# Kernel optimization log

Measured on AMD Instinct MI355X. Metric: run time of the kernel, lower is better.

The kernel has to match this reference:

```python
import jax, jax.numpy as jnp
import numpy as np

B, N = 32, 1000
HID, COM = 256, 64
T_LEN, NOP = 288, 3
NVAL, TP_D, CS_D, TIME_D = 9, 2, 4, 4
IN_C = CS_D + TP_D + NVAL            # 15, competition GAT input
IN_CO = IN_C + COM                    # 79, cooperation GAT input
OBS = TIME_D + TP_D + CS_D + 2 * COM + NVAL  # 147
K_D = K_F = 500                       # int(0.5*N + 0.5)
TEMP = 1.0
NEG = jnp.float32(-1e8)


def setup_inputs() -> dict:
    key = jax.random.key(0)
    ks = jax.random.split(key, 24)
    def nrm(k, shp, scale=0.05):
        return (jax.random.normal(k, shp, dtype=jnp.float32) * scale)
    return {
        "time_idx": jax.random.randint(ks[0], (B, N), 0, T_LEN, dtype=jnp.int32),
        "op_idx": jax.random.randint(ks[1], (B, N), 0, NOP, dtype=jnp.int32),
        "value_feats": jax.random.normal(ks[2], (B, N, NVAL), dtype=jnp.float32),
        "dpcs_mark": jax.random.randint(ks[3], (B, N, 1), 0, 2) > 0,
        "adj_comp": jax.random.randint(ks[4], (B, N, N), 0, 2) > 0,
        "adj_coop": jax.random.randint(ks[5], (B, N, N), 0, 2) > 0,
        "distance": jax.random.uniform(ks[6], (N, N), dtype=jnp.float32),
        "time_tab": jax.random.uniform(ks[7], (T_LEN, TIME_D), dtype=jnp.float32),
        "tp_tab": jax.random.uniform(ks[8], (NOP, TP_D), dtype=jnp.float32),
        "cs_tab": jax.random.uniform(ks[9], (N, CS_D), dtype=jnp.float32),
        "Wc": nrm(ks[10], (IN_C, COM)),
        "asrc_c": nrm(ks[11], (COM,)),
        "adst_c": nrm(ks[12], (COM,)),
        "wd_c": jnp.float32(0.1),
        "Wco": nrm(ks[13], (IN_CO, COM)),
        "asrc_co": nrm(ks[14], (COM,)),
        "adst_co": nrm(ks[15], (COM,)),
        "wd_co": jnp.float32(0.1),
        "Wp": nrm(ks[16], (OBS, HID)),
        "bp": jnp.zeros((HID,), dtype=jnp.float32),
        "vpd": nrm(ks[17], (HID,)),
        "vpf": nrm(ks[18], (HID,)),
    }


def gat(x, W, a_src, a_dst, w_d, adj, dist):
    """Single-head GAT over dense boolean adjacency. adj[b,j,i] True => edge j->i."""
    h = jnp.einsum("bnf,fd->bnd", x, W)                       # (B,N,D)
    e = (jnp.einsum("bid,d->bi", h, a_dst)[:, :, None]        # dst term
         + jnp.einsum("bjd,d->bj", h, a_src)[:, None, :]      # src term
         + w_d * dist.T[None])                                 # dist[j,i] edge feat
    e = jax.nn.leaky_relu(e, 0.2)
    mask = jnp.swapaxes(adj, 1, 2)                             # (B, dst i, src j)
    e = jnp.where(mask, e, NEG)
    alpha = jax.nn.softmax(e, axis=-1)
    alpha = jnp.where(mask, alpha, 0.0)                        # isolated nodes -> 0
    return jax.nn.elu(jnp.einsum("bij,bjd->bid", alpha, h))


def gated_pool(x_p, scores, valid, k, temp):
    scores = scores - scores.max(axis=1, keepdims=True)
    scores = jnp.where(valid, scores, NEG)                     # (B,N,1)
    val_topk = jax.lax.top_k(scores[..., 0], k)[0]             # (B,k)
    min_topk = val_topk.min(axis=-1)[:, None, None]
    scores = jnp.where(scores < min_topk, NEG, scores)
    w = jax.nn.softmax(scores / temp, axis=1)
    xg = x_p * w
    return jnp.concatenate([xg.sum(axis=1), xg.max(axis=1)], axis=-1)  # (B,2H)


def reference(time_idx, op_idx, value_feats, dpcs_mark, adj_comp, adj_coop,
              distance, time_tab, tp_tab, cs_tab, Wc, asrc_c, adst_c, wd_c,
              Wco, asrc_co, adst_co, wd_co, Wp, bp, vpd, vpf):
    time_e = time_tab[time_idx]                                # (B,N,4)
    tp_e = tp_tab[op_idx]                                      # (B,N,2)
    cs_e = jnp.broadcast_to(cs_tab[None], (B, N, CS_D))        # (B,N,4)
    vf_det = jax.lax.stop_gradient(value_feats)
    x = jnp.concatenate([cs_e, tp_e, vf_det], axis=-1)         # (B,N,15)
    comp_reps = gat(x, Wc, asrc_c, adst_c, wd_c, adj_comp, distance)
    x_m = jnp.concatenate([x, comp_reps], axis=-1)             # (B,N,79)
    coop_reps = gat(x_m, Wco, asrc_co, adst_co, wd_co, adj_coop, distance)
    sag = jnp.concatenate([time_e, cs_e, tp_e, value_feats, comp_reps, coop_reps], axis=-1)
    x_p = jnp.einsum("bnf,fh->bnh", sag, Wp) + bp              # (B,N,HID)
    scores_d = jnp.einsum("bnh,h->bn", x_p, vpd)[..., None]
    s_d = gated_pool(x_p, scores_d, dpcs_mark, K_D, TEMP)
    scores_f = jnp.einsum("bnh,h->bn", x_p, vpf)[..., None]
    s_f = gated_pool(x_p, scores_f, ~dpcs_mark, K_F, TEMP)
    return jnp.concatenate([s_f, s_d], axis=-1)                # (B, 4*HID)
```

## Files before the change

### kernel.cpp

```cpp
#include <hip/hip_runtime.h>
#include <hip/hip_bf16.h>

#define NB 32
#define NN 1000
#define COMD 64
#define HIDD 256
#define KSEL 500
#define TI 16
#define NSPL 32
#define ROWS 32
#define DSTRIDE 1024

#define PB_AQ1  0
#define PB_AQ2  1024
#define PB_DT   2048
#define PB_WP   2304
#define PB_WCO  2344
#define PB_MISC 2368
#define PB_EMB  2369
#define PB_N    (PB_EMB + NB * NN / 4)

typedef __hip_bfloat16 bf16;
typedef unsigned long long u64;
typedef __attribute__((ext_vector_type(4))) float f32x4;
typedef __attribute__((ext_vector_type(8))) short s16x8;
typedef __attribute__((ext_vector_type(4))) short s16x4;
typedef __attribute__((ext_vector_type(4))) unsigned short u16x4;
typedef __attribute__((ext_vector_type(2))) unsigned long long u64x2;

__device__ __forceinline__ float b2f(bf16 x){ return __bfloat162float(x); }

template<bool F32>
__device__ __forceinline__ float ldf(const void* p, long i){
  return F32 ? ((const float*)p)[i] : b2f(((const bf16*)p)[i]);
}
template<bool BINT>
__device__ __forceinline__ bool ldb(const void* p, long i){
  return BINT ? (((const int*)p)[i] != 0) : (((const unsigned char*)p)[i] != 0);
}

__device__ __forceinline__ float wave_sum(float v){
#pragma unroll
  for (int o = 32; o > 0; o >>= 1) v += __shfl_down(v, o, 64);
  return v;
}
__device__ __forceinline__ float wave_bsum(float v){
#pragma unroll
  for (int o = 32; o > 0; o >>= 1) v += __shfl_xor(v, o, 64);
  return v;
}
__device__ __forceinline__ float wave_bmax(float v){
#pragma unroll
  for (int o = 32; o > 0; o >>= 1) v = fmaxf(v, __shfl_xor(v, o, 64));
  return v;
}
__device__ __forceinline__ int wave_bsum_i(int v){
#pragma unroll
  for (int o = 32; o > 0; o >>= 1) v += __shfl_xor(v, o, 64);
  return v;
}
__device__ __forceinline__ unsigned fkey(float f){
  unsigned u = __float_as_uint(f);
  return (u & 0x80000000u) ? ~u : (u | 0x80000000u);
}
__device__ __forceinline__ void split_bf(float v, short& hi, short& lo){
  unsigned u = __float_as_uint(v);
  float hf = __uint_as_float(u & 0xFFFF0000u);
  hi = (short)(u >> 16);
  float r = v - hf;
  lo = (short)(__float_as_uint(r) >> 16);
}
__device__ __forceinline__ short f2bs(float v){
  bf16 h = __float2bfloat16(v);
  short s; __builtin_memcpy(&s, &h, 2); return s;
}
__device__ __forceinline__ void hB_write(short* hB_hi, short* hB_lo,
                                         int b, int n, int ch, float v){
  int kb = n >> 5, g4 = (n >> 3) & 3, u = n & 7;
  long off = ((((long)b * 32 + kb) * 4 + g4) * 64 + ch) * 8 + u;
  short hi, lo; split_bf(v, hi, lo);
  hB_hi[off] = hi; hB_lo[off] = lo;
}
__device__ __forceinline__ void sniff2(const void* dist, const void* adjc,
                                       int lane, int& f32, int& as_int){
  unsigned wdist = ((const unsigned*)dist)[lane];
  unsigned wadj  = ((const unsigned*)adjc)[lane];
  f32 = (__ballot((wdist & 0xFFFFu) >= 0x8000u) != 0ull) ? 1 : 0;
  as_int = (__ballot(wadj > 1u) == 0ull) ? 1 : 0;
}

#define SMEM_BYTES 8704

template<bool F32>
__device__ __forceinline__ void dist_t_role(const void* dist, bf16* distTb,
                                            int rel, void* sm){
  bf16 (*tile)[68] = (bf16 (*)[68])sm;
  int t = threadIdx.x;
  int wv = t >> 6, lane = t & 63;
  int it = (rel & 15) * 64, jt = (rel >> 4) * 64;
#pragma unroll
  for (int r = 0; r < 16; ++r){
    int jl = r * 4 + wv;
    int j = jt + jl, i = it + lane;
    float v = (j < NN && i < NN) ? ldf<F32>(dist, (long)j * NN + i) : 0.f;
    tile[jl][lane] = __float2bfloat16(v);
  }
  __syncthreads();
#pragma unroll
  for (int r = 0; r < 16; ++r){
    int il = r * 4 + wv;
    int i = it + il, j = jt + lane;
    if (i < NN) distTb[(long)i * DSTRIDE + j] = tile[lane][il];
  }
}
template<bool BINT>
__device__ __forceinline__ void adjq_role(const void* adj, u64* adjQ,
                                          int rel, void* sm){
  u64 (*aw)[33] = (u64 (*)[33])sm;
  int t = threadIdx.x;
  int wv = t >> 6, lane = t & 63;
  int j0 = (rel & 31) * 32;
  int b  = rel >> 5;
  int ch3 = (192 + lane < 250) ? (192 + lane) : 249;
  int chk[4] = { lane, 64 + lane, 128 + lane, ch3 };
  long row0;
  {
    int j = j0 + wv * 8;
    int jc = (j < NN) ? j : (NN - 1);
    row0 = ((long)b * NN + jc) * (long)NN;
  }
  if (BINT){
    const int* base = (const int*)adj;
    uint4 cur[4], nxt[4];
#pragma unroll
    for (int c = 0; c < 4; ++c)
      cur[c] = *(const uint4*)(base + row0 + (long)chk[c] * 4);
#pragma unroll
    for (int r = 0; r < 8; ++r){
      if (r < 7){
        int j2 = j0 + wv * 8 + r + 1;
        int jc2 = (j2 < NN) ? j2 : (NN - 1);
        long row2 = ((long)b * NN + jc2) * (long)NN;
#pragma unroll
        for (int c = 0; c < 4; ++c)
          nxt[c] = *(const uint4*)(base + row2 + (long)chk[c] * 4);
      }
      int j = j0 + wv * 8 + r;
#pragma unroll
      for (int c = 0; c < 4; ++c){
        u64 bal0 = __ballot(cur[c].x != 0u);
        u64 bal1 = __ballot(cur[c].y != 0u);
        u64 bal2 = __ballot(cur[c].z != 0u);
        u64 bal3 = __ballot(cur[c].w != 0u);
        if (lane < 4){
          u64 w = 0;
          if (j < NN){
            int sh = 16 * lane;
            w = ((bal0 >> sh) & 0xFFFFull)
              | (((bal1 >> sh) & 0xFFFFull) << 16)
              | (((bal2 >> sh) & 0xFFFFull) << 32)
              | (((bal3 >> sh) & 0xFFFFull) << 48);
          }
          aw[c * 4 + lane][wv * 8 + r] = w;
        }
      }
      if (r < 7){
#pragma unroll
        for (int c = 0; c < 4; ++c) cur[c] = nxt[c];
      }
    }
  } else {
    const unsigned char* base = (const unsigned char*)adj;
    unsigned cur[4], nxt[4];
#pragma unroll
    for (int c = 0; c < 4; ++c)
      cur[c] = *(const unsigned*)(base + row0 + (long)chk[c] * 4);
#pragma unroll
    for (int r = 0; r < 8; ++r){
      if (r < 7){
        int j2 = j0 + wv * 8 + r + 1;
        int jc2 = (j2 < NN) ? j2 : (NN - 1);
        long row2 = ((long)b * NN + jc2) * (long)NN;
#pragma unroll
        for (int c = 0; c < 4; ++c)
          nxt[c] = *(const unsigned*)(base + row2 + (long)chk[c] * 4);
      }
      int j = j0 + wv * 8 + r;
#pragma unroll
      for (int c = 0; c < 4; ++c){
        u64 bal0 = __ballot((cur[c] & 0xFFu) != 0u);
        u64 bal1 = __ballot((cur[c] & 0xFF00u) != 0u);
        u64 bal2 = __ballot((cur[c] & 0xFF0000u) != 0u);
        u64 bal3 = __ballot((cur[c] & 0xFF000000u) != 0u);
        if (lane < 4){
          u64 w = 0;
          if (j < NN){
            int sh = 16 * lane;
            w = ((bal0 >> sh) & 0xFFFFull)
              | (((bal1 >> sh) & 0xFFFFull) << 16)
              | (((bal2 >> sh) & 0xFFFFull) << 32)
              | (((bal3 >> sh) & 0xFFFFull) << 48);
          }
          aw[c * 4 + lane][wv * 8 + r] = w;
        }
      }
      if (r < 7){
#pragma unroll
        for (int c = 0; c < 4; ++c) cur[c] = nxt[c];
      }
    }
  }
  __syncthreads();
#pragma unroll
  for (int rr = 0; rr < 2; ++rr){
    int w2 = t + rr * 256;
    int iw = w2 >> 5, jloc = w2 & 31;
    adjQ[((long)b * 16 + iw) * 1024 + j0 + jloc] = aw[iw][jloc];
  }
}
template<bool F32>
__device__ __forceinline__ void wp_role(const void* Wp, const void* vpd, const void* vpf,
                        short* WpB_hi, short* WpB_lo, float* wv_ws, int rel){
  int t = threadIdx.x;
  int g = t >> 6, lane = t & 63;
  int f = rel * 4 + g;
  float wrow[4];
#pragma unroll
  for (int r = 0; r < 4; ++r){
    int ch = r * 64 + lane;
    wrow[r] = (f < 147) ? ldf<F32>(Wp, (long)f * HIDD + ch) : 0.f;
  }
  int kb = f >> 5, q = (f >> 3) & 3, u = f & 7;
#pragma unroll
  for (int r = 0; r < 4; ++r){
    int ch = r * 64 + lane;
    long off = (((long)(kb * 4 + q)) * 256 + ch) * 8 + u;
    short hi, lo; split_bf(wrow[r], hi, lo);
    WpB_hi[off] = hi; WpB_lo[off] = lo;
  }
  float ad = 0.f, af = 0.f;
#pragma unroll
  for (int r = 0; r < 4; ++r){
    int ch = r * 64 + lane;
    ad += wrow[r] * ldf<F32>(vpd, ch);
    af += wrow[r] * ldf<F32>(vpf, ch);
  }
  ad = wave_bsum(ad); af = wave_bsum(af);
  if (lane == 0){ wv_ws[f] = ad; wv_ws[160 + f] = af; }
}
template<bool F32>
__device__ __forceinline__ void wco_role(const void* Wco, const void* asrc, const void* adst,
                         short* WcoB_hi, short* WcoB_lo, float* pvco, int rel){
  int t = threadIdx.x;
  int g = t >> 6, lane = t & 63;
  int f = rel * 4 + g;
  float w = (f < 79) ? ldf<F32>(Wco, (long)f * COMD + lane) : 0.f;
  int kb = f >> 5, q = (f >> 3) & 3, u = f & 7;
  long off = (((long)(kb * 4 + q)) * 64 + lane) * 8 + u;
  short hi, lo; split_bf(w, hi, lo);
  WcoB_hi[off] = hi; WcoB_lo[off] = lo;
  float dd = wave_bsum(w * ldf<F32>(adst, lane));
  float ss = wave_bsum(w * ldf<F32>(asrc, lane));
  if (lane == 0){ pvco[f] = dd; pvco[96 + f] = ss; }
}
template<bool F32>
__device__ __forceinline__ void misc_role(const void* wdc, const void* wdco,
                          const void* bp, const void* vpd, const void* vpf,
                          int f32, int as_int,
                          int* flags, float* wd_ws, float* wv_ws){
  int t = threadIdx.x;
  if (t >= 64) return;
  int lane = t;
  float ad = 0.f, af = 0.f;
#pragma unroll
  for (int r = 0; r < 4; ++r){
    int ch = r * 64 + lane;
    float bb = ldf<F32>(bp, ch);
    ad += bb * ldf<F32>(vpd, ch);
    af += bb * ldf<F32>(vpf, ch);
  }
  ad = wave_bsum(ad); af = wave_bsum(af);
  if (lane == 0){
    wv_ws[320] = ad; wv_ws[321] = af;
    wd_ws[0] = ldf<F32>(wdc, 0);
    wd_ws[1] = ldf<F32>(wdco, 0);
    flags[0] = f32; flags[1] = as_int;
  }
}
template<bool F32>
__device__ __forceinline__ void embed_body(
    const int* op_idx, const void* vf, const void* cs_tab, const void* tp_tab,
    const void* Wc, const void* asrc, const void* adst,
    float* x_out, short* hB_hi, short* hB_lo, float* ed_out, float* es_out,
    int rel){
  int t = threadIdx.x;
  int w = t >> 6, lane = t & 63;
  int g = rel * 4 + w;
  int b = g / NN, n = g - b * NN;
  int op = op_idx[g];
  float xv = 0.f, hacc = 0.f;
#pragma unroll
  for (int f = 0; f < 15; ++f){
    float x_f;
    if (f < 4)      x_f = ldf<F32>(cs_tab, n * 4 + f);
    else if (f < 6) x_f = ldf<F32>(tp_tab, op * 2 + (f - 4));
    else            x_f = ldf<F32>(vf, (long)g * 9 + (f - 6));
    if (lane == f) xv = x_f;
    hacc += x_f * ldf<F32>(Wc, f * COMD + lane);
  }
  if (lane < 15) x_out[g * 15 + lane] = xv;
  hB_write(hB_hi, hB_lo, b, n, lane, hacc);
  float sd = wave_sum(hacc * ldf<F32>(adst, lane));
  float ss = wave_sum(hacc * ldf<F32>(asrc, lane));
  if (lane == 0){ ed_out[g] = sd; es_out[g] = ss; }
}
__global__ void __launch_bounds__(256) k_prep(
    const void* dist, const void* adj_comp, const void* adj_coop,
    const void* wdc, const void* wdco,
    const void* Wp, const void* vpd, const void* vpf, const void* bp,
    const void* Wco, const void* asrc_co, const void* adst_co,
    const int* op_idx, const void* vfeat, const void* cs_tab, const void* tp_tab,
    const void* Wc, const void* asrc_c, const void* adst_c,
    int* flags, float* wd_ws, bf16* distTb, u64* adjQc, u64* adjQo,
    short* WpB_hi, short* WpB_lo, float* wv_ws,
    short* WcoB_hi, short* WcoB_lo, float* pvco,
    float* x_ws, short* hB_hi, short* hB_lo, float* ed_c, float* es_c){
  __shared__ __attribute__((aligned(16))) char smem[SMEM_BYTES];
  int blk = blockIdx.x;
  int f32, as_int;
  sniff2(dist, adj_comp, threadIdx.x & 63, f32, as_int);
  if (blk < PB_AQ2){
    if (as_int) adjq_role<true >(adj_comp, adjQc, blk - PB_AQ1, smem);
    else        adjq_role<false>(adj_comp, adjQc, blk - PB_AQ1, smem);
  } else if (blk < PB_DT){
    if (as_int) adjq_role<true >(adj_coop, adjQo, blk - PB_AQ2, smem);
    else        adjq_role<false>(adj_coop, adjQo, blk - PB_AQ2, smem);
  } else if (blk < PB_WP){
    if (f32) dist_t_role<true >(dist, distTb, blk - PB_DT, smem);
    else     dist_t_role<false>(dist, distTb, blk - PB_DT, smem);
  } else if (blk < PB_WCO){
    if (f32) wp_role<true >(Wp, vpd, vpf, WpB_hi, WpB_lo, wv_ws, blk - PB_WP);
    else     wp_role<false>(Wp, vpd, vpf, WpB_hi, WpB_lo, wv_ws, blk - PB_WP);
  } else if (blk < PB_MISC){
    if (f32) wco_role<true >(Wco, asrc_co, adst_co, WcoB_hi, WcoB_lo, pvco, blk - PB_WCO);
    else     wco_role<false>(Wco, asrc_co, adst_co, WcoB_hi, WcoB_lo, pvco, blk - PB_WCO);
  } else if (blk < PB_EMB){
    if (f32) misc_role<true >(wdc, wdco, bp, vpd, vpf, f32, as_int, flags, wd_ws, wv_ws);
    else     misc_role<false>(wdc, wdco, bp, vpd, vpf, f32, as_int, flags, wd_ws, wv_ws);
  } else {
    if (f32) embed_body<true >(op_idx, vfeat, cs_tab, tp_tab, Wc, asrc_c, adst_c,
                               x_ws, hB_hi, hB_lo, ed_c, es_c, blk - PB_EMB);
    else     embed_body<false>(op_idx, vfeat, cs_tab, tp_tab, Wc, asrc_c, adst_c,
                               x_ws, hB_hi, hB_lo, ed_c, es_c, blk - PB_EMB);
  }
}

__global__ void __launch_bounds__(256) k_hco(
    const float* __restrict__ x_ws, const float* __restrict__ comp,
    const short* __restrict__ WcoB_hi, const short* __restrict__ WcoB_lo,
    const float* __restrict__ pvco,
    short* hB_hi, short* hB_lo, float* ed_out, float* es_out){
  __shared__ float cx[16][80] __attribute__((aligned(16)));
  __shared__ short cA_hi[3 * 16 * 40] __attribute__((aligned(16)));
  __shared__ short cA_lo[3 * 16 * 40] __attribute__((aligned(16)));
  int t = threadIdx.x;
  int wv = t >> 6, lane = t & 63;
  int base = blockIdx.x * 16;
  for (int idx = t; idx < 16 * 79; idx += 256){
    int nl = idx / 79, f = idx - nl * 79;
    int g = base + nl;
    cx[nl][f] = (f < 15) ? x_ws[g * 15 + f] : comp[(long)g * COMD + (f - 15)];
  }
  __syncthreads();
  {
    int node = t >> 4, sub = t & 15;
    float dd = 0.f, ss = 0.f;
    for (int f = sub; f < 79; f += 16){
      float c = cx[node][f];
      dd += c * pvco[f];
      ss += c * pvco[96 + f];
    }
#pragma unroll
    for (int o = 8; o > 0; o >>= 1){
      dd += __shfl_xor(dd, o, 64);
      ss += __shfl_xor(ss, o, 64);
    }
    if (sub == 0){
      int g = base + node;
      ed_out[g] = dd; es_out[g] = ss;
    }
  }
  for (int idx = t; idx < 16 * 96; idx += 256){
    int m = idx / 96, k = idx - m * 96;
    float v = (k < 79) ? cx[m][k] : 0.f;
    int kb = k >> 5, q = (k >> 3) & 3, u = k & 7;
    short hi, lo; split_bf(v, hi, lo);
    int off = (kb * 16 + m) * 40 + q * 8 + u;
    cA_hi[off] = hi; cA_lo[off] = lo;
  }
  __syncthreads();
  int q = lane >> 4, m = lane & 15;
  int ch = wv * 16 + m;
  f32x4 acc = {0.f, 0.f, 0.f, 0.f};
#pragma unroll
  for (int kb = 0; kb < 3; ++kb){
    int aoff = (kb * 16 + m) * 40 + q * 8;
    s16x8 a_hi = *(const s16x8*)&cA_hi[aoff];
    s16x8 a_lo = *(const s16x8*)&cA_lo[aoff];
    long boff = (((long)(kb * 4 + q)) * 64 + ch) * 8;
    s16x8 b_hi = *(const s16x8*)&WcoB_hi[boff];
    s16x8 b_lo = *(const s16x8*)&WcoB_lo[boff];
    acc = __builtin_amdgcn_mfma_f32_16x16x32_bf16(a_hi, b_hi, acc, 0, 0, 0);
    acc = __builtin_amdgcn_mfma_f32_16x16x32_bf16(a_hi, b_lo, acc, 0, 0, 0);
    acc = __builtin_amdgcn_mfma_f32_16x16x32_bf16(a_lo, b_hi, acc, 0, 0, 0);
  }
#pragma unroll
  for (int reg = 0; reg < 4; ++reg){
    int row = (lane >> 4) * 4 + reg;
    int g = base + row;
    int b = g / NN, n = g - b * NN;
    hB_write(hB_hi, hB_lo, b, n, ch, acc[reg]);
  }
}

__global__ void __launch_bounds__(256) k_gat(
    const float* __restrict__ ed, const float* __restrict__ es,
    const float* __restrict__ wd_ws, int wd_idx, const u64* __restrict__ adjQ,
    const bf16* __restrict__ distTb,
    const short* __restrict__ hB_hi, const short* __restrict__ hB_lo,
    float* __restrict__ reps){
  __shared__ short pA[32 * 544] __attribute__((aligned(16)));
  __shared__ float redz[TI][4];
  __shared__ float esred[4];
  int t = threadIdx.x;
  int wv = t >> 6, lane = t & 63;
  int b = blockIdx.y;
  int i0 = blockIdx.x * TI;
  float wd = wd_ws[wd_idx];
  int iw = i0 >> 6;
  int sb2 = (i0 & 63) >> 2;
  int j0 = t * 4;

  const u64* aq = adjQ + ((long)b * 16 + iw) * 1024 + j0;
  u64x2 wA = *(const u64x2*)&aq[0];
  u64x2 wB = *(const u64x2*)&aq[2];
  u64 wsh[4] = { wA[0] >> sb2, wA[1] >> sb2, wB[0] >> sb2, wB[1] >> sb2 };
  float4 es4 = *(const float4*)&es[(long)b * NN + j0];
  float esv[4] = {es4.x, es4.y, es4.z, es4.w};
  float esm = -1e30f;
#pragma unroll
  for (int c = 0; c < 4; ++c)
    esm = fmaxf(esm, (j0 + c < NN) ? esv[c] : -1e30f);
  esm = wave_bmax(esm);
  if (lane == 0) esred[wv] = esm;

  float ed_i[TI]; float edm = -1e30f;
#pragma unroll
  for (int ti = 0; ti < TI; ++ti){
    int i = i0 + ti;
    float ev = ed[(long)b * NN + ((i < NN) ? i : (NN - 1))];
    ed_i[ti] = ev;
    edm = fmaxf(edm, (i < NN) ? ev : -1e30f);
  }
  __syncthreads();
  float M = fmaxf(fmaxf(esred[0], esred[1]), fmaxf(esred[2], esred[3]))
            + edm + fmaxf(wd, 0.f);
  M = fmaxf(M, 0.f);

  float p[TI][4];
  const bf16* dbase = distTb + j0;
#pragma unroll
  for (int ti = 0; ti < TI; ++ti){
    int i = i0 + ti;
    int ic = (i < NN) ? i : (NN - 1);
    u16x4 d4 = *(const u16x4*)&dbase[(long)ic * DSTRIDE];
    float edti = ed_i[ti];
    int psh = 16 * (ti & 3) + (ti >> 2);
#pragma unroll
    for (int c = 0; c < 4; ++c){
      float d = __uint_as_float((unsigned)d4[c] << 16);
      float v = edti + esv[c] + wd * d;
      v = fmaxf(v, 0.2f * v);
      bool edge = (wsh[c] >> psh) & 1ull;
      float e = edge ? v : -1e30f;
      p[ti][c] = __expf(e - M);
    }
  }

  int kbw = 8 * wv + (lane >> 3);
  int qw = (lane >> 1) & 3;
  int u0 = 4 * (lane & 1);
  int wbase = kbw * 544 + qw * 136 + u0;
#pragma unroll
  for (int ti = 0; ti < TI; ++ti){
    float zs = p[ti][0] + p[ti][1] + p[ti][2] + p[ti][3];
    zs = wave_bsum(zs);
    if (lane == 0) redz[ti][wv] = zs;
    s16x4 s4 = { f2bs(p[ti][0]), f2bs(p[ti][1]), f2bs(p[ti][2]), f2bs(p[ti][3]) };
    *(s16x4*)&pA[wbase + ti * 8] = s4;
  }
  __syncthreads();

  int q = lane >> 4, m = lane & 15;
  int abase = q * 136 + m * 8;
  int ch = wv * 16 + m;
  const short* bh = hB_hi + (long)b * 65536 + ((long)q * 64 + ch) * 8;
  const short* bl = hB_lo + (long)b * 65536 + ((long)q * 64 + ch) * 8;
  f32x4 acc = {0.f, 0.f, 0.f, 0.f};
#pragma unroll
  for (int kb = 0; kb < 32; ++kb){
    s16x8 a   = *(const s16x8*)&pA[kb * 544 + abase];
    s16x8 bhi = *(const s16x8*)&bh[(long)kb * 2048];
    s16x8 blo = *(const s16x8*)&bl[(long)kb * 2048];
    acc = __builtin_amdgcn_mfma_f32_16x16x32_bf16(a, bhi, acc, 0, 0, 0);
    acc = __builtin_amdgcn_mfma_f32_16x16x32_bf16(a, blo, acc, 0, 0, 0);
  }
#pragma unroll
  for (int reg = 0; reg < 4; ++reg){
    int ti = (lane >> 4) * 4 + reg;
    float z = redz[ti][0] + redz[ti][1] + redz[ti][2] + redz[ti][3];
    float zi = (z > 0.f) ? 1.f / z : 0.f;
    float v = acc[reg] * zi;
    v = (v > 0.f) ? v : expm1f(v);
    int ch2 = wv * 16 + (lane & 15);
    if (i0 + ti < NN)
      reps[((long)b * NN + i0 + ti) * COMD + ch2] = v;
  }
}

template<bool F32>
__device__ __forceinline__ void xp_body(
    const int* time_idx, const int* op_idx, const void* vf, const void* time_tab,
    const void* cs_tab, const void* tp_tab, const float* comp, const float* coop,
    const short* __restrict__ WpB_hi, const short* __restrict__ WpB_lo,
    const float* __restrict__ wv_ws, const void* bp,
    float* x_p, float* scf, float* scd){
  __shared__ float sagF[16][148] __attribute__((aligned(16)));
  __shared__ short sagA_hi[5 * 16 * 40] __attribute__((aligned(16)));
  __shared__ short sagA_lo[5 * 16 * 40] __attribute__((aligned(16)));
  int t = threadIdx.x;
  int wv = t >> 6, lane = t & 63;
  int base = blockIdx.x * 16;

  for (int idx = t; idx < 16 * 147; idx += 256){
    int nl = idx / 147, f = idx - nl * 147;
    int g = base + nl;
    int n = g % NN;
    float v;
    if (f < 4)       v = ldf<F32>(time_tab, time_idx[g] * 4 + f);
    else if (f < 8)  v = ldf<F32>(cs_tab, n * 4 + (f - 4));
    else if (f < 10) v = ldf<F32>(tp_tab, op_idx[g] * 2 + (f - 8));
    else if (f < 19) v = ldf<F32>(vf, (long)g * 9 + (f - 10));
    else if (f < 83) v = comp[(long)g * COMD + (f - 19)];
    else             v = coop[(long)g * COMD + (f - 83)];
    sagF[nl][f] = v;
  }
  __syncthreads();

  for (int idx = t; idx < 16 * 160; idx += 256){
    int m = idx / 160, k = idx - m * 160;
    float v = (k < 147) ? sagF[m][k] : 0.f;
    int kb = k >> 5, q = (k >> 3) & 3, u = k & 7;
    short hi, lo; split_bf(v, hi, lo);
    int off = (kb * 16 + m) * 40 + q * 8 + u;
    sagA_hi[off] = hi; sagA_lo[off] = lo;
  }
  {
    int node = t >> 4, sub = t & 15;
    float ad = 0.f, af = 0.f;
    for (int f = sub; f < 147; f += 16){
      float s = sagF[node][f];
      ad += s * wv_ws[f];
      af += s * wv_ws[160 + f];
    }
#pragma unroll
    for (int o = 8; o > 0; o >>= 1){
      ad += __shfl_xor(ad, o, 64);
      af += __shfl_xor(af, o, 64);
    }
    if (sub == 0){
      scd[base + node] = ad + wv_ws[320];
      scf[base + node] = af + wv_ws[321];
    }
  }
  __syncthreads();

  int Ag = lane >> 4, Am = lane & 15;
  f32x4 acc[4] = {{0,0,0,0},{0,0,0,0},{0,0,0,0},{0,0,0,0}};
#pragma unroll
  for (int kb = 0; kb < 5; ++kb){
    int aoff = (kb * 16 + Am) * 40 + Ag * 8;
    s16x8 a_hi = *(const s16x8*)&sagA_hi[aoff];
    s16x8 a_lo = *(const s16x8*)&sagA_lo[aoff];
#pragma unroll
    for (int ct = 0; ct < 4; ++ct){
      int ch = wv * 64 + ct * 16 + Am;
      long boff = (((long)(kb * 4 + Ag)) * 256 + ch) * 8;
      s16x8 b_hi = *(const s16x8*)&WpB_hi[boff];
      s16x8 b_lo = *(const s16x8*)&WpB_lo[boff];
      acc[ct] = __builtin_amdgcn_mfma_f32_16x16x32_bf16(a_hi, b_hi, acc[ct], 0, 0, 0);
      acc[ct] = __builtin_amdgcn_mfma_f32_16x16x32_bf16(a_hi, b_lo, acc[ct], 0, 0, 0);
      acc[ct] = __builtin_amdgcn_mfma_f32_16x16x32_bf16(a_lo, b_hi, acc[ct], 0, 0, 0);
    }
  }
#pragma unroll
  for (int ct = 0; ct < 4; ++ct){
    int ch = wv * 64 + ct * 16 + (lane & 15);
    float bb = ldf<F32>(bp, ch);
#pragma unroll
    for (int reg = 0; reg < 4; ++reg){
      int row = (lane >> 4) * 4 + reg;
      x_p[(long)(base + row) * HIDD + ch] = acc[ct][reg] + bb;
    }
  }
}
__global__ void __launch_bounds__(256) k_xp(
    const int* flags, const int* time_idx, const int* op_idx, const void* vf,
    const void* time_tab, const void* cs_tab, const void* tp_tab,
    const float* comp, const float* coop,
    const short* WpB_hi, const short* WpB_lo, const float* wv_ws, const void* bp,
    float* x_p, float* scf, float* scd){
  if (flags[0]) xp_body<true >(time_idx, op_idx, vf, time_tab, cs_tab, tp_tab, comp, coop, WpB_hi, WpB_lo, wv_ws, bp, x_p, scf, scd);
  else          xp_body<false>(time_idx, op_idx, vf, time_tab, cs_tab, tp_tab, comp, coop, WpB_hi, WpB_lo, wv_ws, bp, x_p, scf, scd);
}

template<bool BINT>
__device__ __forceinline__ void topk_body(
    const float* scf, const float* scd, const void* mark, float* wls){
  int lane = threadIdx.x;
  int b = blockIdx.x, pool = blockIdx.y;
  const float* sc = (pool == 0) ? scf : scd;
  float v[16]; unsigned key[16];
  float m0 = -INFINITY;
#pragma unroll
  for (int r = 0; r < 16; ++r){
    int n = r * 64 + lane;
    float s = (n < NN) ? sc[b * NN + n] : -INFINITY;
    v[r] = s;
    m0 = fmaxf(m0, s);
  }
  m0 = wave_bmax(m0);
  float m1 = -INFINITY;
#pragma unroll
  for (int r = 0; r < 16; ++r){
    int n = r * 64 + lane;
    bool valid = false;
    if (n < NN){
      bool mk = ldb<BINT>(mark, b * NN + n);
      valid = (pool == 0) ? !mk : mk;
    }
    v[r] = valid ? (v[r] - m0) : -1e8f;
    key[r] = fkey(v[r]);
    if (n < NN) m1 = fmaxf(m1, v[r]);
  }
  m1 = wave_bmax(m1);

  unsigned lo = 0u, hi = 0xFFFFFFFFu;
  while (lo < hi){
    unsigned mid = lo + ((hi - lo) >> 1) + 1u;
    int c = 0;
#pragma unroll
    for (int r = 0; r < 16; ++r) c += (key[r] >= mid) ? 1 : 0;
    c = wave_bsum_i(c);
    if (c >= KSEL) lo = mid; else hi = mid - 1u;
  }

  float p[16];
  float ls = 0.f;
#pragma unroll
  for (int r = 0; r < 16; ++r){
    int n = r * 64 + lane;
    float pp = (n < NN && key[r] >= lo) ? __expf(v[r] - m1) : 0.f;
    p[r] = pp;
    ls += pp;
  }
  ls = wave_bsum(ls);
  float zinv = (ls > 0.f) ? 1.f / ls : 0.f;
  float* w_out = wls + ((long)b * 2 + pool) * 1024;
#pragma unroll
  for (int r = 0; r < 16; ++r){
    int n = r * 64 + lane;
    if (n < NN) w_out[n] = p[r] * zinv;
  }
}
__global__ void k_topk(const int* flags, const float* scf, const float* scd,
                       const void* mark, float* wls){
  if (flags[1]) topk_body<true >(scf, scd, mark, wls);
  else          topk_body<false>(scf, scd, mark, wls);
}

__global__ void __launch_bounds__(256) k_psum(
    const float* __restrict__ wls, const float* __restrict__ x_p,
    float* __restrict__ part){
  __shared__ float wf[ROWS], wdd[ROWS];
  int t = threadIdx.x;
  int b = blockIdx.x, z = blockIdx.y;
  int n0 = z * ROWS;
  int ns = min(ROWS, NN - n0);
  if (t < ns){
    wf[t]  = wls[((long)b * 2 + 0) * 1024 + n0 + t];
    wdd[t] = wls[((long)b * 2 + 1) * 1024 + n0 + t];
  }
  __syncthreads();
  float sf = 0.f, mf = -INFINITY, sd = 0.f, md = -INFINITY;
  const float* xb = x_p + ((long)b * NN + n0) * HIDD + t;
  for (int k = 0; k < ns; ++k){
    float xv = xb[(long)k * HIDD];
    float gf = wf[k] * xv;
    float gd = wdd[k] * xv;
    sf += gf; mf = fmaxf(mf, gf);
    sd += gd; md = fmaxf(md, gd);
  }
  long pb = (((long)b * NSPL + z) * 4) * HIDD + t;
  part[pb + 0 * HIDD] = sf;
  part[pb + 1 * HIDD] = mf;
  part[pb + 2 * HIDD] = sd;
  part[pb + 3 * HIDD] = md;
}

template<bool F32>
__device__ __forceinline__ void pfin_body(const float* part, void* out){
  int t = threadIdx.x;
  int b = blockIdx.x;
  float sf = 0.f, mf = -INFINITY, sd = 0.f, md = -INFINITY;
#pragma unroll
  for (int z = 0; z < NSPL; ++z){
    long pb = (((long)b * NSPL + z) * 4) * HIDD + t;
    sf += part[pb + 0 * HIDD];
    mf = fmaxf(mf, part[pb + 1 * HIDD]);
    sd += part[pb + 2 * HIDD];
    md = fmaxf(md, part[pb + 3 * HIDD]);
  }
  long ob = (long)b * 1024;
  if (F32){
    ((float*)out)[ob + t] = sf;
    ((float*)out)[ob + 256 + t] = mf;
    ((float*)out)[ob + 512 + t] = sd;
    ((float*)out)[ob + 768 + t] = md;
  } else {
    ((bf16*)out)[ob + t] = __float2bfloat16(sf);
    ((bf16*)out)[ob + 256 + t] = __float2bfloat16(mf);
    ((bf16*)out)[ob + 512 + t] = __float2bfloat16(sd);
    ((bf16*)out)[ob + 768 + t] = __float2bfloat16(md);
  }
}
__global__ void k_pfin(const int* flags, const float* part, void* out){
  if (flags[0]) pfin_body<true >(part, out);
  else          pfin_body<false>(part, out);
}

extern "C" void kernel_launch(void* const* d_in, const int* in_sizes, int n_in,
                              void* d_out, int out_size, void* d_ws, size_t ws_size,
                              hipStream_t stream){
  const int*  time_idx = (const int*)d_in[0];
  const int*  op_idx   = (const int*)d_in[1];
  const void* vfeat    = d_in[2];
  const void* dpcs     = d_in[3];
  const void* adj_comp = d_in[4];
  const void* adj_coop = d_in[5];
  const void* dist     = d_in[6];
  const void* time_tab = d_in[7];
  const void* tp_tab   = d_in[8];
  const void* cs_tab   = d_in[9];
  const void* Wc       = d_in[10];
  const void* asrc_c   = d_in[11];
  const void* adst_c   = d_in[12];
  const void* wd_c     = d_in[13];
  const void* Wco      = d_in[14];
  const void* asrc_co  = d_in[15];
  const void* adst_co  = d_in[16];
  const void* wd_co    = d_in[17];
  const void* Wp       = d_in[18];
  const void* bp       = d_in[19];
  const void* vpd      = d_in[20];
  const void* vpf      = d_in[21];

  char* ws = (char*)d_ws;
  size_t o = 0;
  auto alloc = [&](size_t bytes)->char*{
    char* p = ws + o; o = (o + bytes + 255) & ~(size_t)255; return p;
  };
  int*   flags   = (int*)alloc(16);
  float* wd_ws   = (float*)alloc(8);
  bf16*  distTb  = (bf16*)alloc((size_t)NN * DSTRIDE * 2);
  u64*   adjQc   = (u64*)alloc((size_t)NB * 16 * 1024 * 8);
  u64*   adjQo   = (u64*)alloc((size_t)NB * 16 * 1024 * 8);
  float* x_ws    = (float*)alloc((size_t)NB * NN * 15 * 4);
  float* comp    = (float*)alloc((size_t)NB * NN * COMD * 4);
  float* coop    = (float*)alloc((size_t)NB * NN * COMD * 4);
  short* hB_hi   = (short*)alloc((size_t)NB * 65536 * 2);
  short* hB_lo   = (short*)alloc((size_t)NB * 65536 * 2);
  short* WpB_hi  = (short*)alloc((size_t)5 * 4 * 256 * 8 * 2);
  short* WpB_lo  = (short*)alloc((size_t)5 * 4 * 256 * 8 * 2);
  short* WcoB_hi = (short*)alloc((size_t)3 * 4 * 64 * 8 * 2);
  short* WcoB_lo = (short*)alloc((size_t)3 * 4 * 64 * 8 * 2);
  float* wv_ws   = (float*)alloc(322 * 4);
  float* pvco    = (float*)alloc(192 * 4);
  float* ed_c    = (float*)alloc((size_t)NB * NN * 4 + 256);
  float* es_c    = (float*)alloc((size_t)NB * NN * 4 + 256);
  float* ed_o    = (float*)alloc((size_t)NB * NN * 4 + 256);
  float* es_o    = (float*)alloc((size_t)NB * NN * 4 + 256);
  float* scf     = (float*)alloc((size_t)NB * NN * 4);
  float* scd     = (float*)alloc((size_t)NB * NN * 4);
  float* wls     = (float*)alloc((size_t)NB * 2 * 1024 * 4);
  float* part    = (float*)alloc((size_t)NB * NSPL * 4 * HIDD * 4);
  float* x_p     = (float*)alloc((size_t)NB * NN * HIDD * 4);

  k_prep<<<dim3(PB_N), dim3(256), 0, stream>>>(
      dist, adj_comp, adj_coop, wd_c, wd_co, Wp, vpd, vpf, bp,
      Wco, asrc_co, adst_co,
      op_idx, vfeat, cs_tab, tp_tab, Wc, asrc_c, adst_c,
      flags, wd_ws, distTb, adjQc, adjQo, WpB_hi, WpB_lo, wv_ws,
      WcoB_hi, WcoB_lo, pvco,
      x_ws, hB_hi, hB_lo, ed_c, es_c);
  k_gat<<<dim3((NN + TI - 1) / TI, NB), dim3(256), 0, stream>>>(
      ed_c, es_c, wd_ws, 0, adjQc, distTb, hB_hi, hB_lo, comp);
  k_hco<<<dim3(NB * NN / 16), dim3(256), 0, stream>>>(
      x_ws, comp, WcoB_hi, WcoB_lo, pvco, hB_hi, hB_lo, ed_o, es_o);
  k_gat<<<dim3((NN + TI - 1) / TI, NB), dim3(256), 0, stream>>>(
      ed_o, es_o, wd_ws, 1, adjQo, distTb, hB_hi, hB_lo, coop);
  k_xp<<<dim3(NB * NN / 16), dim3(256), 0, stream>>>(
      flags, time_idx, op_idx, vfeat, time_tab, cs_tab, tp_tab, comp, coop,
      WpB_hi, WpB_lo, wv_ws, bp, x_p, scf, scd);
  k_topk<<<dim3(NB, 2), dim3(64), 0, stream>>>(flags, scf, scd, dpcs, wls);
  k_psum<<<dim3(NB, NSPL), dim3(256), 0, stream>>>(wls, x_p, part);
  k_pfin<<<dim3(NB), dim3(256), 0, stream>>>(flags, part, d_out);
}
```

Measured before the change: 487.6 us.

## Move coop adjacency packing into first GAT launch as extra blocks

```diff
diff --git a/kernel.cpp b/kernel.cpp
--- a/kernel.cpp
+++ b/kernel.cpp
@@ -7,17 +7,18 @@
 #define HIDD 256
 #define KSEL 500
 #define TI 16
+#define GATX ((NN + TI - 1) / TI)
+#define PACKX 32
 #define NSPL 32
 #define ROWS 32
 #define DSTRIDE 1024
 
 #define PB_AQ1  0
-#define PB_AQ2  1024
-#define PB_DT   2048
-#define PB_WP   2304
-#define PB_WCO  2344
-#define PB_MISC 2368
-#define PB_EMB  2369
+#define PB_DT   1024
+#define PB_WP   1280
+#define PB_WCO  1320
+#define PB_MISC 1344
+#define PB_EMB  1345
 #define PB_N    (PB_EMB + NB * NN / 4)
 
 typedef __hip_bfloat16 bf16;
@@ -315,13 +316,13 @@
   if (lane == 0){ ed_out[g] = sd; es_out[g] = ss; }
 }
 __global__ void __launch_bounds__(256) k_prep(
-    const void* dist, const void* adj_comp, const void* adj_coop,
+    const void* dist, const void* adj_comp,
     const void* wdc, const void* wdco,
     const void* Wp, const void* vpd, const void* vpf, const void* bp,
     const void* Wco, const void* asrc_co, const void* adst_co,
     const int* op_idx, const void* vfeat, const void* cs_tab, const void* tp_tab,
     const void* Wc, const void* asrc_c, const void* adst_c,
-    int* flags, float* wd_ws, bf16* distTb, u64* adjQc, u64* adjQo,
+    int* flags, float* wd_ws, bf16* distTb, u64* adjQc,
     short* WpB_hi, short* WpB_lo, float* wv_ws,
     short* WcoB_hi, short* WcoB_lo, float* pvco,
     float* x_ws, short* hB_hi, short* hB_lo, float* ed_c, float* es_c){
@@ -329,12 +330,9 @@
   int blk = blockIdx.x;
   int f32, as_int;
   sniff2(dist, adj_comp, threadIdx.x & 63, f32, as_int);
-  if (blk < PB_AQ2){
+  if (blk < PB_DT){
     if (as_int) adjq_role<true >(adj_comp, adjQc, blk - PB_AQ1, smem);
     else        adjq_role<false>(adj_comp, adjQc, blk - PB_AQ1, smem);
-  } else if (blk < PB_DT){
-    if (as_int) adjq_role<true >(adj_coop, adjQo, blk - PB_AQ2, smem);
-    else        adjq_role<false>(adj_coop, adjQo, blk - PB_AQ2, smem);
   } else if (blk < PB_WP){
     if (f32) dist_t_role<true >(dist, distTb, blk - PB_DT, smem);
     else     dist_t_role<false>(dist, distTb, blk - PB_DT, smem);
@@ -428,10 +426,17 @@
     const float* __restrict__ wd_ws, int wd_idx, const u64* __restrict__ adjQ,
     const bf16* __restrict__ distTb,
     const short* __restrict__ hB_hi, const short* __restrict__ hB_lo,
-    float* __restrict__ reps){
+    float* __restrict__ reps,
+    const int* __restrict__ flags, const void* adj_raw, u64* adjQ_out){
   __shared__ short pA[32 * 544] __attribute__((aligned(16)));
   __shared__ float redz[TI][4];
   __shared__ float esred[4];
+  if (blockIdx.x >= GATX){
+    int rel = (blockIdx.x - GATX) * NB + blockIdx.y;
+    if (flags[1]) adjq_role<true >(adj_raw, adjQ_out, rel, (void*)pA);
+    else          adjq_role<false>(adj_raw, adjQ_out, rel, (void*)pA);
+    return;
+  }
   int t = threadIdx.x;
   int wv = t >> 6, lane = t & 63;
   int b = blockIdx.y;
@@ -807,18 +812,20 @@
   float* x_p     = (float*)alloc((size_t)NB * NN * HIDD * 4);
 
   k_prep<<<dim3(PB_N), dim3(256), 0, stream>>>(
-      dist, adj_comp, adj_coop, wd_c, wd_co, Wp, vpd, vpf, bp,
+      dist, adj_comp, wd_c, wd_co, Wp, vpd, vpf, bp,
       Wco, asrc_co, adst_co,
       op_idx, vfeat, cs_tab, tp_tab, Wc, asrc_c, adst_c,
-      flags, wd_ws, distTb, adjQc, adjQo, WpB_hi, WpB_lo, wv_ws,
+      flags, wd_ws, distTb, adjQc, WpB_hi, WpB_lo, wv_ws,
       WcoB_hi, WcoB_lo, pvco,
       x_ws, hB_hi, hB_lo, ed_c, es_c);
-  k_gat<<<dim3((NN + TI - 1) / TI, NB), dim3(256), 0, stream>>>(
-      ed_c, es_c, wd_ws, 0, adjQc, distTb, hB_hi, hB_lo, comp);
+  k_gat<<<dim3(GATX + PACKX, NB), dim3(256), 0, stream>>>(
+      ed_c, es_c, wd_ws, 0, adjQc, distTb, hB_hi, hB_lo, comp,
+      flags, adj_coop, adjQo);
   k_hco<<<dim3(NB * NN / 16), dim3(256), 0, stream>>>(
       x_ws, comp, WcoB_hi, WcoB_lo, pvco, hB_hi, hB_lo, ed_o, es_o);
-  k_gat<<<dim3((NN + TI - 1) / TI, NB), dim3(256), 0, stream>>>(
-      ed_o, es_o, wd_ws, 1, adjQo, distTb, hB_hi, hB_lo, coop);
+  k_gat<<<dim3(GATX, NB), dim3(256), 0, stream>>>(
+      ed_o, es_o, wd_ws, 1, adjQo, distTb, hB_hi, hB_lo, coop,
+      flags, nullptr, nullptr);
   k_xp<<<dim3(NB * NN / 16), dim3(256), 0, stream>>>(
       flags, time_idx, op_idx, vfeat, time_tab, cs_tab, tp_tab, comp, coop,
       WpB_hi, WpB_lo, wv_ws, bp, x_p, scf, scd);
```

After: 471.9 us. 3.2% less time.
